# Performance work log

Measured on AMD Instinct MI355X. Metric: run time of the kernel, lower is better.

## Reference

```python
import jax, jax.numpy as jnp
import numpy as np

# Constants hard-coded in Phi_r.forward / Prior_SPDE (dx=dy=dt=1, tau=1, Qs=I)
KAPPA = 0.33
GAMMA = 1.0
BETA = 25.0
DT = 1.0


def _apply_A(u, H11, H12, H22):
    """Anisotropic SPDE operator A u = kappa^2 u - div(H grad u).

    u: [B, T, Y, X] field; H11/H12/H22: [B, Y, X] diffusion tensor entries.
    Centered 9-point stencil, zero (Dirichlet) boundary via zero padding --
    this is the dense-grid equivalent of the sparse DiffOperator assembly.
    """
    up = jnp.pad(u, ((0, 0), (0, 0), (1, 1), (1, 1)))
    c = up[:, :, 1:-1, 1:-1]
    uxx = up[:, :, 1:-1, 2:] - 2.0 * c + up[:, :, 1:-1, :-2]
    uyy = up[:, :, 2:, 1:-1] - 2.0 * c + up[:, :, :-2, 1:-1]
    uxy = 0.25 * (up[:, :, 2:, 2:] - up[:, :, 2:, :-2]
                  - up[:, :, :-2, 2:] + up[:, :, :-2, :-2])
    div = (H11[:, None] * uxx + 2.0 * H12[:, None] * uxy
           + H22[:, None] * uyy)
    return (KAPPA * KAPPA) * u - div


def setup_inputs() -> dict:
    key = jax.random.key(0)
    state = jax.random.normal(key, (8, 9, 512, 512), dtype=jnp.float32)
    return {"state": state}


def reference(state):
    # state: [n_b, n_t+2, n_y, n_x]
    n_b, n_tp2, n_y, n_x = state.shape
    n_t = n_tp2 - 2
    x = state[:, :n_t]            # [B, T, Y, X]
    vx = state[:, n_t]            # [B, Y, X]
    vy = state[:, n_t + 1]

    # H = gamma*I + beta * v v^T per node
    H11 = GAMMA + BETA * vx * vx
    H12 = BETA * vx * vy
    H22 = GAMMA + BETA * vy * vy

    # Apply operator to every time slice at once; M = I + dt*A
    Ax = _apply_A(x, H11, H12, H22)   # [B, T, Y, X]
    Mx = x + DT * Ax

    sq = lambda a: jnp.sum(a * a, axis=(-2, -1))  # reduce spatial dims
    nx = sq(x)    # [B, T]
    nM = sq(Mx)   # [B, T]

    # Block-tridiagonal precision Q (tau=1 -> Qs_tilde = I):
    #   Q00 = A^T A + 0.05 I + I            -> ||A x0||^2 + 1.05 ||x0||^2
    #   Qii = M^T M + I  (1 <= i <= T-2)    -> ||M xi||^2 + ||xi||^2
    #   Q(T-1,T-1) = M^T M                  -> ||M x_{T-1}||^2
    #   Q(i,i+1) = -M, Q(i+1,i) = -M^T      -> -2 xi . (M x_{i+1})
    cross = jnp.sum(x[:, : n_t - 1] * Mx[:, 1:], axis=(-2, -1)).sum(axis=-1)
    q = (sq(Ax[:, 0]) + 1.05 * nx[:, 0]
         + nM[:, 1:].sum(axis=1)
         + nx[:, 1 : n_t - 1].sum(axis=1)
         - 2.0 * cross)
    return q  # [n_b] quadratic forms x^T Q x
```

## Files before the change

### kernel.cpp

```cpp
#include <hip/hip_runtime.h>

#define N 512
#define KAPPA2 0.1089f
#define GAMMA  1.0f
#define BETA   25.0f

__device__ __forceinline__ void loadspan10(const float* __restrict__ p, int lane,
                                           float s[10]) {
    const float4 A = *reinterpret_cast<const float4*>(p);
    const float4 B = *reinterpret_cast<const float4*>(p + 4);
    s[1] = A.x; s[2] = A.y; s[3] = A.z; s[4] = A.w;
    s[5] = B.x; s[6] = B.y; s[7] = B.z; s[8] = B.w;
    const float lw = __shfl_up(B.w, 1, 64);
    const float rx = __shfl_down(A.x, 1, 64);
    s[0] = (lane == 0)  ? 0.0f : lw;
    s[9] = (lane == 63) ? 0.0f : rx;
}

__device__ __forceinline__ void zero10(float s[10]) {
    #pragma unroll
    for (int j = 0; j < 10; ++j) s[j] = 0.0f;
}

__global__ __launch_bounds__(64, 7) void phi_q_stage1(const float* __restrict__ state,
                                                      float* __restrict__ ws) {
    const int bid  = blockIdx.x;
    const int b    = bid & 7;
    const int yt   = bid >> 3;
    const int y    = yt / 7;
    const int t    = yt - y * 7;
    const int lane = threadIdx.x;

    const size_t slice  = (size_t)N * N;
    const float* base   = state + (size_t)b * 9 * slice;
    const size_t rowoff = (size_t)y * N + lane * 8;

    const bool ym = (y > 0), yp = (y < N - 1);

    const float* u = base + (size_t)t * slice;
    float sm[10], sc[10], su[10];
    loadspan10(u + rowoff, lane, sc);
    if (ym) loadspan10(u + rowoff - N, lane, sm);
    else    zero10(sm);
    if (yp) loadspan10(u + rowoff + N, lane, su);
    else    zero10(su);

    const float4 vxA = *reinterpret_cast<const float4*>(base + 7 * slice + rowoff);
    const float4 vxB = *reinterpret_cast<const float4*>(base + 7 * slice + rowoff + 4);
    const float4 vyA = *reinterpret_cast<const float4*>(base + 8 * slice + rowoff);
    const float4 vyB = *reinterpret_cast<const float4*>(base + 8 * slice + rowoff + 4);
    const float vxs[8] = {vxA.x, vxA.y, vxA.z, vxA.w, vxB.x, vxB.y, vxB.z, vxB.w};
    const float vys[8] = {vyA.x, vyA.y, vyA.z, vyA.w, vyB.x, vyB.y, vyB.z, vyB.w};

    float xp8[8];
    if (t > 0) {
        const float* up = u - slice;
        const float4 XA = *reinterpret_cast<const float4*>(up + rowoff);
        const float4 XB = *reinterpret_cast<const float4*>(up + rowoff + 4);
        xp8[0] = XA.x; xp8[1] = XA.y; xp8[2] = XA.z; xp8[3] = XA.w;
        xp8[4] = XB.x; xp8[5] = XB.y; xp8[6] = XB.z; xp8[7] = XB.w;
    } else {
        #pragma unroll
        for (int j = 0; j < 8; ++j) xp8[j] = 0.0f;
    }

    float q = 0.0f;
    #pragma unroll
    for (int j = 0; j < 8; ++j) {
        const float c   = sc[j + 1];
        const float uxx = sc[j] + sc[j + 2] - 2.0f * c;
        const float uyy = sm[j + 1] + su[j + 1] - 2.0f * c;
        const float uxy = 0.25f * (su[j + 2] - su[j] - sm[j + 2] + sm[j]);
        const float vx = vxs[j], vy = vys[j];
        const float div = (GAMMA + BETA * vx * vx) * uxx
                        + (2.0f * BETA * vx * vy) * uxy
                        + (GAMMA + BETA * vy * vy) * uyy;
        const float Ax  = KAPPA2 * c - div;
        if (t == 0) {
            q += Ax * Ax + 1.05f * c * c;
        } else {
            const float Mx = c + Ax;
            q += Mx * Mx - 2.0f * xp8[j] * Mx;
            if (t < 6) q += c * c;
        }
    }

    #pragma unroll
    for (int off = 32; off > 0; off >>= 1)
        q += __shfl_down(q, off, 64);

    if (lane == 0) ws[b * 3584 + yt] = q;
}

__global__ __launch_bounds__(256) void phi_q_stage2(const float* __restrict__ ws,
                                                    float* __restrict__ out) {
    const int b = blockIdx.x;
    const float* p = ws + b * 3584;
    float v = 0.0f;
    #pragma unroll
    for (int k = 0; k < 14; ++k)
        v += p[k * 256 + threadIdx.x];

    #pragma unroll
    for (int off = 32; off > 0; off >>= 1)
        v += __shfl_down(v, off, 64);

    __shared__ float sred[4];
    const int lane = threadIdx.x & 63;
    const int wid  = threadIdx.x >> 6;
    if (lane == 0) sred[wid] = v;
    __syncthreads();
    if (threadIdx.x == 0) out[b] = sred[0] + sred[1] + sred[2] + sred[3];
}

extern "C" void kernel_launch(void* const* d_in, const int* in_sizes, int n_in,
                              void* d_out, int out_size, void* d_ws, size_t ws_size,
                              hipStream_t stream) {
    const float* state = (const float*)d_in[0];
    float* out = (float*)d_out;
    float* ws  = (float*)d_ws;

    phi_q_stage1<<<28672, 64, 0, stream>>>(state, ws);
    phi_q_stage2<<<8, 256, 0, stream>>>(ws, out);
}
```

Measured before the change: 24.54 us.

## Process 8-row strips per wavefront with rolling row registers

Each 64-thread block now walks an 8-row strip and rotates its above, centre and below row registers, so every row of u is loaded once per strip instead of three times. This cuts the grid eightfold and shrinks the partial-sum workspace and the second-stage reduction to match. The t branches become multiplier coefficients, which removes divergence at the cost of a little extra arithmetic. Having fewer, longer blocks reduces parallelism and latency hiding, and the vx, vy and previous-slice loads stay serialized inside the row loop.

```diff
diff --git a/kernel.cpp b/kernel.cpp
--- a/kernel.cpp
+++ b/kernel.cpp
@@ -1,6 +1,7 @@
 #include <hip/hip_runtime.h>
 
 #define N 512
+#define SLICE (512 * 512)
 #define KAPPA2 0.1089f
 #define GAMMA  1.0f
 #define BETA   25.0f
@@ -22,84 +23,90 @@
     for (int j = 0; j < 10; ++j) s[j] = 0.0f;
 }
 
-__global__ __launch_bounds__(64, 7) void phi_q_stage1(const float* __restrict__ state,
-                                                      float* __restrict__ ws) {
+__global__ __launch_bounds__(64) void phi_q_stage1(const float* __restrict__ state,
+                                                   float* __restrict__ ws) {
     const int bid  = blockIdx.x;
     const int b    = bid & 7;
-    const int yt   = bid >> 3;
-    const int y    = yt / 7;
-    const int t    = yt - y * 7;
+    const int g    = bid >> 3;
+    const int strip = g / 7;
+    const int t    = g - strip * 7;
+    const int y0   = strip * 8;
     const int lane = threadIdx.x;
+    const int xo   = lane * 8;
 
-    const size_t slice  = (size_t)N * N;
-    const float* base   = state + (size_t)b * 9 * slice;
-    const size_t rowoff = (size_t)y * N + lane * 8;
+    const float* base = state + (size_t)b * 9 * SLICE;
+    const float* u    = base + (size_t)t * SLICE;
+    const float* vxp  = base + 7 * SLICE;
+    const float* vyp  = base + 8 * SLICE;
+    const float* xprv = u - SLICE;
 
-    const bool ym = (y > 0), yp = (y < N - 1);
+    const float m     = (t == 0) ? 0.0f : 1.0f;
+    const float ccoef = (t == 0) ? 1.05f : ((t < 6) ? 1.0f : 0.0f);
 
-    const float* u = base + (size_t)t * slice;
     float sm[10], sc[10], su[10];
-    loadspan10(u + rowoff, lane, sc);
-    if (ym) loadspan10(u + rowoff - N, lane, sm);
-    else    zero10(sm);
-    if (yp) loadspan10(u + rowoff + N, lane, su);
-    else    zero10(su);
-
-    const float4 vxA = *reinterpret_cast<const float4*>(base + 7 * slice + rowoff);
-    const float4 vxB = *reinterpret_cast<const float4*>(base + 7 * slice + rowoff + 4);
-    const float4 vyA = *reinterpret_cast<const float4*>(base + 8 * slice + rowoff);
-    const float4 vyB = *reinterpret_cast<const float4*>(base + 8 * slice + rowoff + 4);
-    const float vxs[8] = {vxA.x, vxA.y, vxA.z, vxA.w, vxB.x, vxB.y, vxB.z, vxB.w};
-    const float vys[8] = {vyA.x, vyA.y, vyA.z, vyA.w, vyB.x, vyB.y, vyB.z, vyB.w};
-
-    float xp8[8];
-    if (t > 0) {
-        const float* up = u - slice;
-        const float4 XA = *reinterpret_cast<const float4*>(up + rowoff);
-        const float4 XB = *reinterpret_cast<const float4*>(up + rowoff + 4);
-        xp8[0] = XA.x; xp8[1] = XA.y; xp8[2] = XA.z; xp8[3] = XA.w;
-        xp8[4] = XB.x; xp8[5] = XB.y; xp8[6] = XB.z; xp8[7] = XB.w;
-    } else {
-        #pragma unroll
-        for (int j = 0; j < 8; ++j) xp8[j] = 0.0f;
-    }
+    if (y0 > 0) loadspan10(u + (size_t)(y0 - 1) * N + xo, lane, sm);
+    else        zero10(sm);
+    loadspan10(u + (size_t)y0 * N + xo, lane, sc);
 
     float q = 0.0f;
     #pragma unroll
-    for (int j = 0; j < 8; ++j) {
-        const float c   = sc[j + 1];
-        const float uxx = sc[j] + sc[j + 2] - 2.0f * c;
-        const float uyy = sm[j + 1] + su[j + 1] - 2.0f * c;
-        const float uxy = 0.25f * (su[j + 2] - su[j] - sm[j + 2] + sm[j]);
-        const float vx = vxs[j], vy = vys[j];
-        const float div = (GAMMA + BETA * vx * vx) * uxx
-                        + (2.0f * BETA * vx * vy) * uxy
-                        + (GAMMA + BETA * vy * vy) * uyy;
-        const float Ax  = KAPPA2 * c - div;
-        if (t == 0) {
-            q += Ax * Ax + 1.05f * c * c;
+    for (int k = 0; k < 8; ++k) {
+        const int y = y0 + k;
+        const size_t ro = (size_t)y * N + xo;
+
+        if (y + 1 < N) loadspan10(u + ro + N, lane, su);
+        else           zero10(su);
+
+        const float4 vxA = *reinterpret_cast<const float4*>(vxp + ro);
+        const float4 vxB = *reinterpret_cast<const float4*>(vxp + ro + 4);
+        const float4 vyA = *reinterpret_cast<const float4*>(vyp + ro);
+        const float4 vyB = *reinterpret_cast<const float4*>(vyp + ro + 4);
+        const float vxs[8] = {vxA.x, vxA.y, vxA.z, vxA.w, vxB.x, vxB.y, vxB.z, vxB.w};
+        const float vys[8] = {vyA.x, vyA.y, vyA.z, vyA.w, vyB.x, vyB.y, vyB.z, vyB.w};
+
+        float xp8[8];
+        if (t > 0) {
+            const float4 XA = *reinterpret_cast<const float4*>(xprv + ro);
+            const float4 XB = *reinterpret_cast<const float4*>(xprv + ro + 4);
+            xp8[0] = XA.x; xp8[1] = XA.y; xp8[2] = XA.z; xp8[3] = XA.w;
+            xp8[4] = XB.x; xp8[5] = XB.y; xp8[6] = XB.z; xp8[7] = XB.w;
         } else {
-            const float Mx = c + Ax;
-            q += Mx * Mx - 2.0f * xp8[j] * Mx;
-            if (t < 6) q += c * c;
+            #pragma unroll
+            for (int j = 0; j < 8; ++j) xp8[j] = 0.0f;
         }
+
+        #pragma unroll
+        for (int j = 0; j < 8; ++j) {
+            const float c   = sc[j + 1];
+            const float uxx = sc[j] + sc[j + 2] - 2.0f * c;
+            const float uyy = sm[j + 1] + su[j + 1] - 2.0f * c;
+            const float uxy = 0.25f * (su[j + 2] - su[j] - sm[j + 2] + sm[j]);
+            const float vx = vxs[j], vy = vys[j];
+            const float div = (GAMMA + BETA * vx * vx) * uxx
+                            + (2.0f * BETA * vx * vy) * uxy
+                            + (GAMMA + BETA * vy * vy) * uyy;
+            const float Ax  = KAPPA2 * c - div;
+            const float val = m * c + Ax;
+            q += val * val - 2.0f * xp8[j] * val + ccoef * c * c;
+        }
+
+        #pragma unroll
+        for (int i = 0; i < 10; ++i) { sm[i] = sc[i]; sc[i] = su[i]; }
     }
 
     #pragma unroll
     for (int off = 32; off > 0; off >>= 1)
         q += __shfl_down(q, off, 64);
 
-    if (lane == 0) ws[b * 3584 + yt] = q;
+    if (lane == 0) ws[b * 448 + g] = q;
 }
 
 __global__ __launch_bounds__(256) void phi_q_stage2(const float* __restrict__ ws,
                                                     float* __restrict__ out) {
     const int b = blockIdx.x;
-    const float* p = ws + b * 3584;
-    float v = 0.0f;
-    #pragma unroll
-    for (int k = 0; k < 14; ++k)
-        v += p[k * 256 + threadIdx.x];
+    const float* p = ws + b * 448;
+    float v = p[threadIdx.x];
+    if (threadIdx.x < 192) v += p[256 + threadIdx.x];
 
     #pragma unroll
     for (int off = 32; off > 0; off >>= 1)
@@ -120,6 +127,6 @@
     float* out = (float*)d_out;
     float* ws  = (float*)d_ws;
 
-    phi_q_stage1<<<28672, 64, 0, stream>>>(state, ws);
+    phi_q_stage1<<<3584, 64, 0, stream>>>(state, ws);
     phi_q_stage2<<<8, 256, 0, stream>>>(ws, out);
 }
```

Measured after the change: 37.92 us. +54.5%, slower.
